# Kernel tuning notes

Measured on AMD Instinct MI355X. Metric: run time of the kernel, lower is better.

Reference implementation:

```python
import jax, jax.numpy as jnp
import numpy as np

B, S_WP, D_BERT = 64, 512, 768
NUM_WORDS = 256   # max words per sentence (segment count for scatter-mean)
H = 256           # LSTM hidden dim
A_MAX, K_MAX = 8, 4
N_LABELS = 4


def setup_inputs() -> dict:
    key = jax.random.key(0)
    ks = jax.random.split(key, 16)
    s = lambda shape, k, scale=0.05: jax.random.normal(k, shape, jnp.float32) * scale
    inp = {
        "embeddings": jax.random.normal(ks[0], (B, S_WP, D_BERT), jnp.float32),
        "mask": jnp.sort(jax.random.randint(ks[1], (B, S_WP), 0, NUM_WORDS), axis=-1),
        "aspect_idxs": jax.random.randint(ks[2], (B, A_MAX, K_MAX), 0, NUM_WORDS - 2),
        "w_ih_f": s((4 * H, D_BERT), ks[3]),
        "w_hh_f": s((4 * H, H), ks[4]),
        "b_ih_f": s((4 * H,), ks[5]),
        "b_hh_f": s((4 * H,), ks[6]),
        "w_ih_r": s((4 * H, D_BERT), ks[7]),
        "w_hh_r": s((4 * H, H), ks[8]),
        "b_ih_r": s((4 * H,), ks[9]),
        "b_hh_r": s((4 * H,), ks[10]),
        "fc1_w": s((H, 4 * H), ks[11]),
        "fc1_b": s((H,), ks[12]),
        "fc2_w": s((N_LABELS, H), ks[13]),
        "fc2_b": s((N_LABELS,), ks[14]),
    }
    return inp


def _lstm_dir(x, w_ih, w_hh, b_ih, b_hh, reverse):
    # x: [B, S, D] -> [B, S, H]; PyTorch gate order i, f, g, o.
    b, _, _ = x.shape
    h_dim = w_hh.shape[1]
    xg = jnp.einsum('bsd,gd->bsg', x, w_ih) + b_ih  # precompute input gates

    def step(carry, xg_t):
        h, c = carry
        g = xg_t + h @ w_hh.T + b_hh
        i, f, gg, o = jnp.split(g, 4, axis=-1)
        c = jax.nn.sigmoid(f) * c + jax.nn.sigmoid(i) * jnp.tanh(gg)
        h = jax.nn.sigmoid(o) * jnp.tanh(c)
        return (h, c), h

    init = (jnp.zeros((b, h_dim), x.dtype), jnp.zeros((b, h_dim), x.dtype))
    _, hs = jax.lax.scan(step, init, xg.transpose(1, 0, 2), reverse=reverse)
    return hs.transpose(1, 0, 2)


def _forward(embeddings, mask, aspect_idxs, w_ih_f, w_hh_f, b_ih_f, b_hh_f,
             w_ih_r, w_hh_r, b_ih_r, b_hh_r, fc1_w, fc1_b, fc2_w, fc2_b):
    # batch_scatter_mean: pool wordpieces into words via segment mean.
    seg_sum = jax.vmap(lambda e, m: jax.ops.segment_sum(e, m, num_segments=NUM_WORDS))(embeddings, mask)
    cnt = jax.vmap(lambda m: jax.ops.segment_sum(jnp.ones(m.shape, embeddings.dtype), m, num_segments=NUM_WORDS))(mask)
    words = seg_sum / jnp.maximum(cnt, 1.0)[..., None]  # [B, NUM_WORDS, D_BERT]

    # Bidirectional LSTM (dropout is identity in eval).
    h_f = _lstm_dir(words, w_ih_f, w_hh_f, b_ih_f, b_hh_f, reverse=False)
    h_r = _lstm_dir(words, w_ih_r, w_hh_r, b_ih_r, b_hh_r, reverse=True)
    out = jnp.concatenate([h_f, h_r], axis=-1)  # [B, S_words, 2H]

    b, s, hd = out.shape
    sent_mean = out.mean(axis=1)  # [B, 2H] (mean over full padded sequence, as original)

    # Ragged aspect gather-mean: sent_out[idxs + 1].mean(0), -1 pads masked out.
    tok_valid = (aspect_idxs >= 0).astype(out.dtype)              # [B, A, K]
    idx = jnp.clip(aspect_idxs, 0, s - 2) + 1                     # [B, A, K]
    gathered = jnp.take_along_axis(out, idx.reshape(b, -1, 1), axis=1)  # [B, A*K, 2H]
    gathered = gathered.reshape(b, A_MAX, K_MAX, hd)
    n_tok = tok_valid.sum(-1)                                     # [B, A]
    asp_mean = (gathered * tok_valid[..., None]).sum(2) / jnp.maximum(n_tok, 1.0)[..., None]

    valid = (n_tok > 0)[..., None]
    sent_b = jnp.broadcast_to(sent_mean[:, None, :], (b, A_MAX, hd))
    emb = jnp.where(valid, jnp.concatenate([sent_b, asp_mean], axis=-1), 0.0)  # [B, A, 4H]

    flat = emb.reshape(b * A_MAX, 2 * hd)
    h1 = jax.nn.relu(flat @ fc1_w.T + fc1_b)
    logits = h1 @ fc2_w.T + fc2_b
    return logits.reshape(b, A_MAX, -1)


def reference(embeddings, mask, aspect_idxs, w_ih_f, w_hh_f, b_ih_f, b_hh_f,
              w_ih_r, w_hh_r, b_ih_r, b_hh_r, fc1_w, fc1_b, fc2_w, fc2_b):
    return _forward(embeddings, mask, aspect_idxs, w_ih_f, w_hh_f, b_ih_f, b_hh_f,
                    w_ih_r, w_hh_r, b_ih_r, b_hh_r, fc1_w, fc1_b, fc2_w, fc2_b)
```

## Files before the change

kernel.cpp:

```cpp
#include <hip/hip_runtime.h>
#include <hip/hip_bf16.h>
#include <hip/hip_fp16.h>

#define B_   64
#define SWP  512
#define D_   768
#define W_   256
#define H_   256
#define G4   1024
#define N2   2048
#define M_   16384
#define A_   8
#define KK_  4

typedef __attribute__((ext_vector_type(4))) float f32x4;
typedef __attribute__((ext_vector_type(8))) short bf16x8;
typedef _Float16 __attribute__((ext_vector_type(2))) h2_t;

#define KR2 100
#define NCH 14

__device__ __forceinline__ void gload_lds16(const void* g, void* l) {
  __builtin_amdgcn_global_load_lds((const __attribute__((address_space(1))) void*)g,
                                   (__attribute__((address_space(3))) void*)l, 16, 0, 0);
}

__device__ __forceinline__ float sigm(float x) { return 1.f / (1.f + __expf(-x)); }
__device__ __forceinline__ float tanh_(float x) { return 1.f - 2.f / (1.f + __expf(2.f * x)); }

__device__ __forceinline__ float dot2acc(h2_t w, h2_t h, float acc) {
#if __has_builtin(__builtin_amdgcn_fdot2)
  return __builtin_amdgcn_fdot2(w, h, acc, false);
#else
  return acc + (float)w[0] * (float)h[0] + (float)w[1] * (float)h[1];
#endif
}

__device__ __forceinline__ h2_t bc_h2(unsigned int v) {
  union { unsigned int u; h2_t h; } cvt;
  cvt.u = v;
  return cvt.h;
}

__global__ __launch_bounds__(256) void k_words(const float* __restrict__ emb,
                                               const int* __restrict__ mask,
                                               __hip_bfloat16* __restrict__ words) {
  const int b = blockIdx.x >> 8;
  const int w = blockIdx.x & 255;
  const int tid = threadIdx.x;
  __shared__ int m[SWP];
  m[tid] = mask[b * SWP + tid];
  m[tid + 256] = mask[b * SWP + 256 + tid];
  __syncthreads();
  int lo = 0, hi = SWP;
  while (lo < hi) { int mid = (lo + hi) >> 1; if (m[mid] < w) lo = mid + 1; else hi = mid; }
  int lo2 = lo, hi2 = SWP;
  while (lo2 < hi2) { int mid = (lo2 + hi2) >> 1; if (m[mid] < w + 1) lo2 = mid + 1; else hi2 = mid; }
  const int cnt = lo2 - lo;
  const float inv = (cnt > 0) ? 1.f / (float)cnt : 0.f;
  float s0 = 0.f, s1 = 0.f, s2 = 0.f;
  for (int s = lo; s < lo2; ++s) {
    const float* row = emb + ((size_t)b * SWP + s) * D_;
    s0 += row[tid]; s1 += row[tid + 256]; s2 += row[tid + 512];
  }
  __hip_bfloat16* o = words + ((size_t)b * W_ + w) * D_;
  o[tid]       = __float2bfloat16(s0 * inv);
  o[tid + 256] = __float2bfloat16(s1 * inv);
  o[tid + 512] = __float2bfloat16(s2 * inv);
}

__global__ __launch_bounds__(256) void k_prep_wih(const float* __restrict__ wf, const float* __restrict__ wr,
                                                  const float* __restrict__ bihf, const float* __restrict__ bhhf,
                                                  const float* __restrict__ bihr, const float* __restrict__ bhhr,
                                                  __hip_bfloat16* __restrict__ wih, float* __restrict__ bias) {
  const int i = blockIdx.x * 256 + threadIdx.x;
  const int n = i / D_;
  const int k = i - n * D_;
  const float v = (n < G4) ? wf[n * D_ + k] : wr[(n - G4) * D_ + k];
  wih[i] = __float2bfloat16(v);
  if (i < N2) {
    bias[i] = (i < G4) ? (bihf[i] + bhhf[i]) : (bihr[i - G4] + bhhr[i - G4]);
  }
}

__global__ __launch_bounds__(256) void k_prep_whh(const float* __restrict__ whf,
                                                  const float* __restrict__ whr,
                                                  h2_t* __restrict__ whhP) {
  const int i = blockIdx.x * 256 + threadIdx.x;
  const int d = i >> 17;
  const int kk = (i >> 10) & 127;
  const int r = i & 1023;
  const float* w = d ? whr : whf;
  h2_t v;
  v[0] = (_Float16)w[r * H_ + 2 * kk];
  v[1] = (_Float16)w[r * H_ + 2 * kk + 1];
  whhP[i] = v;
}

__global__ __launch_bounds__(256) void k_gemm_xg(const __hip_bfloat16* __restrict__ A,
                                                 const __hip_bfloat16* __restrict__ Wt,
                                                 const float* __restrict__ bias,
                                                 _Float16* __restrict__ C) {
  const int bm = blockIdx.y * 128;
  const int bn = blockIdx.x * 128;
  __shared__ __hip_bfloat16 As[128 * 32];
  __shared__ __hip_bfloat16 Bs[128 * 32];
  const int tid = threadIdx.x;
  const int lane = tid & 63;
  const int wave = tid >> 6;
  const int wm = (wave >> 1) * 64;
  const int wn = (wave & 1) * 64;
  const int l15 = lane & 15;
  const int l4 = lane >> 4;
  const int row_a = tid >> 2;
  const int chunk = tid & 3;
  f32x4 acc[4][4] = {};
  for (int k0 = 0; k0 < D_; k0 += 32) {
    const __hip_bfloat16* ga  = A  + (size_t)(bm + row_a) * D_ + k0 + chunk * 8;
    const __hip_bfloat16* ga2 = A  + (size_t)(bm + 64 + row_a) * D_ + k0 + chunk * 8;
    const __hip_bfloat16* gb  = Wt + (size_t)(bn + row_a) * D_ + k0 + chunk * 8;
    const __hip_bfloat16* gb2 = Wt + (size_t)(bn + 64 + row_a) * D_ + k0 + chunk * 8;
    gload_lds16(ga,  As + tid * 8);
    gload_lds16(ga2, As + 2048 + tid * 8);
    gload_lds16(gb,  Bs + tid * 8);
    gload_lds16(gb2, Bs + 2048 + tid * 8);
    __syncthreads();
    bf16x8 af[4], bf[4];
#pragma unroll
    for (int i = 0; i < 4; ++i) {
      af[i] = *(const bf16x8*)(As + (wm + i * 16 + l15) * 32 + l4 * 8);
      bf[i] = *(const bf16x8*)(Bs + (wn + i * 16 + l15) * 32 + l4 * 8);
    }
#pragma unroll
    for (int i = 0; i < 4; ++i)
#pragma unroll
      for (int j = 0; j < 4; ++j)
        acc[i][j] = __builtin_amdgcn_mfma_f32_16x16x32_bf16(af[i], bf[j], acc[i][j], 0, 0, 0);
    __syncthreads();
  }
#pragma unroll
  for (int i = 0; i < 4; ++i) {
    const int m = bm + wm + i * 16 + l4 * 4;
#pragma unroll
    for (int j = 0; j < 4; ++j) {
      const int n = bn + wn + j * 16 + l15;
      const float bs = bias[n];
#pragma unroll
      for (int r = 0; r < 4; ++r)
        C[(size_t)(m + r) * N2 + n] = (_Float16)(acc[i][j][r] + bs);
    }
  }
}

__global__ __launch_bounds__(512)
__attribute__((amdgpu_waves_per_eu(2, 2)))
void k_lstm(const _Float16* __restrict__ xg,
            const h2_t* __restrict__ whhP,
            float* __restrict__ out) {
  const int bx = blockIdx.x;
  const int d = bx & 1;
  const int b = bx >> 1;
  const int t = threadIdx.x;
  const int u = t & 255;
  const bool low = (t < 256);
  const int r1 = low ? u : (256 + u);
  const int r2 = r1 + 512;

  __shared__ __align__(16) _Float16 hbuf[256];
  __shared__ __align__(16) h2_t wlds[NCH][512][4];
  __shared__ float fo[256][2];

  const h2_t* wp = whhP + (size_t)d * (128 * 1024);

  unsigned wr1[KR2], wr2[KR2];
#pragma unroll
  for (int kk = 0; kk < KR2; ++kk) {
    wr1[kk] = *(const unsigned*)&wp[kk * 1024 + r1];
    wr2[kk] = *(const unsigned*)&wp[kk * 1024 + r2];
  }
#pragma unroll
  for (int kk = 0; kk < KR2; ++kk) {
    asm volatile("" : "+v"(wr1[kk]));
    asm volatile("" : "+v"(wr2[kk]));
  }

#pragma unroll
  for (int c = 0; c < NCH; ++c) {
    const int row = (c < 7) ? r1 : r2;
    const int kb = KR2 + (c % 7) * 4;
    f32x4 v;
#pragma unroll
    for (int q = 0; q < 4; ++q)
      ((h2_t*)&v)[q] = wp[(kb + q) * 1024 + row];
    *(f32x4*)&wlds[c][t][0] = v;
  }
  if (t < 256) hbuf[t] = (_Float16)0.f;
  __syncthreads();

  float c_state = 0.f;
#pragma unroll 1
  for (int step = 0; step < W_; ++step) {
    const int tt = d ? (W_ - 1 - step) : step;
    const _Float16* xrow = xg + ((size_t)b * W_ + tt) * N2 + d * G4;
    const float xv1 = (float)xrow[r1];
    const float xv2 = (float)xrow[r2];
    float a1a = 0.f, a1b = 0.f, a2a = 0.f, a2b = 0.f;
    if (step > 0) {
      const f32x4* hb4 = (const f32x4*)&hbuf[0];
#pragma unroll
      for (int c = 0; c < 25; ++c) {
        const f32x4 hv = hb4[c];
        const h2_t* hp = (const h2_t*)&hv;
        a1a = dot2acc(bc_h2(wr1[c * 4 + 0]), hp[0], a1a);
        a1b = dot2acc(bc_h2(wr1[c * 4 + 1]), hp[1], a1b);
        a2a = dot2acc(bc_h2(wr2[c * 4 + 0]), hp[0], a2a);
        a2b = dot2acc(bc_h2(wr2[c * 4 + 1]), hp[1], a2b);
        a1a = dot2acc(bc_h2(wr1[c * 4 + 2]), hp[2], a1a);
        a1b = dot2acc(bc_h2(wr1[c * 4 + 3]), hp[3], a1b);
        a2a = dot2acc(bc_h2(wr2[c * 4 + 2]), hp[2], a2a);
        a2b = dot2acc(bc_h2(wr2[c * 4 + 3]), hp[3], a2b);
      }
#pragma unroll
      for (int j = 0; j < 7; ++j) {
        const f32x4 hv = hb4[25 + j];
        const f32x4 w1v = *(const f32x4*)&wlds[j][t][0];
        const f32x4 w2v = *(const f32x4*)&wlds[7 + j][t][0];
        const h2_t* hp = (const h2_t*)&hv;
        const h2_t* w1p = (const h2_t*)&w1v;
        const h2_t* w2p = (const h2_t*)&w2v;
        a1a = dot2acc(w1p[0], hp[0], a1a);
        a1b = dot2acc(w1p[1], hp[1], a1b);
        a2a = dot2acc(w2p[0], hp[0], a2a);
        a2b = dot2acc(w2p[1], hp[1], a2b);
        a1a = dot2acc(w1p[2], hp[2], a1a);
        a1b = dot2acc(w1p[3], hp[3], a1b);
        a2a = dot2acc(w2p[2], hp[2], a2a);
        a2b = dot2acc(w2p[3], hp[3], a2b);
      }
    }
    const float a1 = a1a + a1b + xv1;
    const float a2 = a2a + a2b + xv2;
    if (!low) { fo[u][0] = a1; fo[u][1] = a2; }
    __syncthreads();
    if (low) {
      const float ig = sigm(a1);
      const float gg = tanh_(a2);
      const float fg = sigm(fo[u][0]);
      const float og = sigm(fo[u][1]);
      c_state = fg * c_state + ig * gg;
      const float h = og * tanh_(c_state);
      out[((size_t)b * W_ + tt) * 512 + d * 256 + u] = h;
      hbuf[u] = (_Float16)h;
    }
    __syncthreads();
  }
}

__global__ __launch_bounds__(256) void k_head(const float* __restrict__ out,
                                              const int* __restrict__ aidx,
                                              const float* __restrict__ fc1w,
                                              const float* __restrict__ fc1b,
                                              const float* __restrict__ fc2w,
                                              const float* __restrict__ fc2b,
                                              float* __restrict__ logits) {
  const int b = blockIdx.x;
  const int t = threadIdx.x;
  __shared__ float emb[A_][1024];
  __shared__ float h1[A_][256];
  __shared__ float sent[512];
  const float* ob = out + (size_t)b * W_ * 512;
  float s0 = 0.f, s1 = 0.f;
  for (int tt = 0; tt < W_; ++tt) {
    s0 += ob[tt * 512 + t];
    s1 += ob[tt * 512 + 256 + t];
  }
  sent[t] = s0 * (1.f / 256.f);
  sent[t + 256] = s1 * (1.f / 256.f);
  __syncthreads();
  for (int a = 0; a < A_; ++a) {
    int nv = 0;
    float m0 = 0.f, m1 = 0.f;
    for (int k = 0; k < KK_; ++k) {
      const int idx = aidx[(b * A_ + a) * KK_ + k];
      if (idx >= 0) {
        const int tt = min(idx, W_ - 2) + 1;
        m0 += ob[tt * 512 + t];
        m1 += ob[tt * 512 + 256 + t];
        nv++;
      }
    }
    const float inv = nv > 0 ? 1.f / (float)nv : 0.f;
    const bool valid = nv > 0;
    emb[a][t]        = valid ? sent[t] : 0.f;
    emb[a][t + 256]  = valid ? sent[t + 256] : 0.f;
    emb[a][512 + t]       = m0 * inv;
    emb[a][512 + 256 + t] = m1 * inv;
  }
  __syncthreads();
  {
    float acc[A_];
#pragma unroll
    for (int a = 0; a < A_; ++a) acc[a] = fc1b[t];
    const float* wrow = fc1w + (size_t)t * 1024;
    for (int j = 0; j < 1024; j += 4) {
      const float4 w = *(const float4*)(wrow + j);
#pragma unroll
      for (int a = 0; a < A_; ++a) {
        const float4 e = *(const float4*)(&emb[a][j]);
        acc[a] += w.x * e.x + w.y * e.y + w.z * e.z + w.w * e.w;
      }
    }
#pragma unroll
    for (int a = 0; a < A_; ++a) h1[a][t] = fmaxf(acc[a], 0.f);
  }
  __syncthreads();
  if (t < A_ * 4) {
    const int a = t >> 2, l = t & 3;
    float acc = fc2b[l];
    const float* w = fc2w + l * 256;
    for (int j = 0; j < 256; ++j) acc += w[j] * h1[a][j];
    logits[(b * A_ + a) * 4 + l] = acc;
  }
}

extern "C" void kernel_launch(void* const* d_in, const int* in_sizes, int n_in,
                              void* d_out, int out_size, void* d_ws, size_t ws_size,
                              hipStream_t stream) {
  const float* emb  = (const float*)d_in[0];
  const int*   mask = (const int*)d_in[1];
  const int*   aidx = (const int*)d_in[2];
  const float* wihf = (const float*)d_in[3];
  const float* whhf = (const float*)d_in[4];
  const float* bihf = (const float*)d_in[5];
  const float* bhhf = (const float*)d_in[6];
  const float* wihr = (const float*)d_in[7];
  const float* whhr = (const float*)d_in[8];
  const float* bihr = (const float*)d_in[9];
  const float* bhhr = (const float*)d_in[10];
  const float* fc1w = (const float*)d_in[11];
  const float* fc1b = (const float*)d_in[12];
  const float* fc2w = (const float*)d_in[13];
  const float* fc2b = (const float*)d_in[14];
  float* logits = (float*)d_out;

  char* ws = (char*)d_ws;
  size_t off = 0;
  auto alloc = [&](size_t bytes) -> void* {
    void* p = ws + off;
    off += (bytes + 255) & ~(size_t)255;
    return p;
  };
  __hip_bfloat16* words = (__hip_bfloat16*)alloc((size_t)M_ * D_ * 2);
  _Float16*       xg    = (_Float16*)alloc((size_t)M_ * N2 * 2);
  __hip_bfloat16* wih   = (__hip_bfloat16*)alloc((size_t)N2 * D_ * 2);
  float*          bias  = (float*)alloc((size_t)N2 * 4);
  h2_t*           whhP  = (h2_t*)alloc((size_t)2 * 128 * 1024 * 4);
  float*          outh  = (float*)alloc((size_t)B_ * W_ * 512 * 4);

  k_words<<<B_ * W_, 256, 0, stream>>>(emb, mask, words);
  k_prep_wih<<<(N2 * D_) / 256, 256, 0, stream>>>(wihf, wihr, bihf, bhhf, bihr, bhhr, wih, bias);
  k_prep_whh<<<(2 * 128 * 1024) / 256, 256, 0, stream>>>(whhf, whhr, whhP);
  dim3 gg(N2 / 128, M_ / 128);
  k_gemm_xg<<<gg, 256, 0, stream>>>(words, wih, bias, xg);
  k_lstm<<<B_ * 2, 512, 0, stream>>>(xg, whhP, outh);
  k_head<<<B_, 256, 0, stream>>>(outh, aidx, fc1w, fc1b, fc2w, fc2b, logits);
}
```

Measured before the change: 659.7 us.

## Hold recurrent weights in AGPRs and broadcast hidden state via readlane

The LSTM recurrent kernel now keeps 96 of 128 packed weight pairs per row in accumulation registers (AGPRs) instead of VGPRs, and moves the rest to a larger LDS staging array. The hidden state is no longer read from LDS as 16-byte vectors. Each lane loads one packed pair, and the values are broadcast with readlane into scalar operands for the dot products. This targets LDS read traffic and VGPR pressure on the per-step critical path. The cost is an extra accvgpr read per weight and serialized readlane instructions.

Measured after the change: 2.064 ms. 213% more time.

```diff
diff --git a/kernel.cpp b/kernel.cpp
--- a/kernel.cpp
+++ b/kernel.cpp
@@ -17,8 +17,8 @@
 typedef __attribute__((ext_vector_type(8))) short bf16x8;
 typedef _Float16 __attribute__((ext_vector_type(2))) h2_t;
 
-#define KR2 100
-#define NCH 14
+#define KA2 96
+#define KL2 32
 
 __device__ __forceinline__ void gload_lds16(const void* g, void* l) {
   __builtin_amdgcn_global_load_lds((const __attribute__((address_space(1))) void*)g,
@@ -162,32 +162,30 @@
   const int b = bx >> 1;
   const int t = threadIdx.x;
   const int u = t & 255;
+  const int l = t & 63;
   const bool low = (t < 256);
   const int r1 = low ? u : (256 + u);
   const int r2 = r1 + 512;
 
   __shared__ __align__(16) _Float16 hbuf[256];
-  __shared__ __align__(16) h2_t wlds[NCH][512][4];
+  __shared__ __align__(16) h2_t wlds[16][512][4];
   __shared__ float fo[256][2];
 
   const h2_t* wp = whhP + (size_t)d * (128 * 1024);
 
-  unsigned wr1[KR2], wr2[KR2];
-#pragma unroll
-  for (int kk = 0; kk < KR2; ++kk) {
-    wr1[kk] = *(const unsigned*)&wp[kk * 1024 + r1];
-    wr2[kk] = *(const unsigned*)&wp[kk * 1024 + r2];
-  }
-#pragma unroll
-  for (int kk = 0; kk < KR2; ++kk) {
-    asm volatile("" : "+v"(wr1[kk]));
-    asm volatile("" : "+v"(wr2[kk]));
-  }
-
-#pragma unroll
-  for (int c = 0; c < NCH; ++c) {
-    const int row = (c < 7) ? r1 : r2;
-    const int kb = KR2 + (c % 7) * 4;
+  unsigned ag1[KA2], ag2[KA2];
+#pragma unroll
+  for (int kk = 0; kk < KA2; ++kk) {
+    unsigned t1 = *(const unsigned*)&wp[kk * 1024 + r1];
+    unsigned t2 = *(const unsigned*)&wp[kk * 1024 + r2];
+    asm volatile("v_accvgpr_write_b32 %0, %1" : "=a"(ag1[kk]) : "v"(t1));
+    asm volatile("v_accvgpr_write_b32 %0, %1" : "=a"(ag2[kk]) : "v"(t2));
+  }
+
+#pragma unroll
+  for (int c = 0; c < 16; ++c) {
+    const int row = (c < 8) ? r1 : r2;
+    const int kb = KA2 + (c & 7) * 4;
     f32x4 v;
 #pragma unroll
     for (int q = 0; q < 4; ++q)
@@ -206,36 +204,53 @@
     const float xv2 = (float)xrow[r2];
     float a1a = 0.f, a1b = 0.f, a2a = 0.f, a2b = 0.f;
     if (step > 0) {
-      const f32x4* hb4 = (const f32x4*)&hbuf[0];
-#pragma unroll
-      for (int c = 0; c < 25; ++c) {
-        const f32x4 hv = hb4[c];
-        const h2_t* hp = (const h2_t*)&hv;
-        a1a = dot2acc(bc_h2(wr1[c * 4 + 0]), hp[0], a1a);
-        a1b = dot2acc(bc_h2(wr1[c * 4 + 1]), hp[1], a1b);
-        a2a = dot2acc(bc_h2(wr2[c * 4 + 0]), hp[0], a2a);
-        a2b = dot2acc(bc_h2(wr2[c * 4 + 1]), hp[1], a2b);
-        a1a = dot2acc(bc_h2(wr1[c * 4 + 2]), hp[2], a1a);
-        a1b = dot2acc(bc_h2(wr1[c * 4 + 3]), hp[3], a1b);
-        a2a = dot2acc(bc_h2(wr2[c * 4 + 2]), hp[2], a2a);
-        a2b = dot2acc(bc_h2(wr2[c * 4 + 3]), hp[3], a2b);
-      }
-#pragma unroll
-      for (int j = 0; j < 7; ++j) {
-        const f32x4 hv = hb4[25 + j];
+      const unsigned hA = *(const unsigned*)&hbuf[2 * l];
+      const unsigned hB = *(const unsigned*)&hbuf[128 + 2 * l];
+#pragma unroll
+      for (int k = 0; k < 64; k += 2) {
+        unsigned w1a, w2a, w1b, w2b;
+        asm volatile("v_accvgpr_read_b32 %0, %1" : "=v"(w1a) : "a"(ag1[k]));
+        asm volatile("v_accvgpr_read_b32 %0, %1" : "=v"(w2a) : "a"(ag2[k]));
+        const h2_t h0 = bc_h2(__builtin_amdgcn_readlane(hA, k));
+        a1a = dot2acc(bc_h2(w1a), h0, a1a);
+        a2a = dot2acc(bc_h2(w2a), h0, a2a);
+        asm volatile("v_accvgpr_read_b32 %0, %1" : "=v"(w1b) : "a"(ag1[k + 1]));
+        asm volatile("v_accvgpr_read_b32 %0, %1" : "=v"(w2b) : "a"(ag2[k + 1]));
+        const h2_t h1 = bc_h2(__builtin_amdgcn_readlane(hA, k + 1));
+        a1b = dot2acc(bc_h2(w1b), h1, a1b);
+        a2b = dot2acc(bc_h2(w2b), h1, a2b);
+      }
+#pragma unroll
+      for (int k = 0; k < 32; k += 2) {
+        unsigned w1a, w2a, w1b, w2b;
+        asm volatile("v_accvgpr_read_b32 %0, %1" : "=v"(w1a) : "a"(ag1[64 + k]));
+        asm volatile("v_accvgpr_read_b32 %0, %1" : "=v"(w2a) : "a"(ag2[64 + k]));
+        const h2_t h0 = bc_h2(__builtin_amdgcn_readlane(hB, k));
+        a1a = dot2acc(bc_h2(w1a), h0, a1a);
+        a2a = dot2acc(bc_h2(w2a), h0, a2a);
+        asm volatile("v_accvgpr_read_b32 %0, %1" : "=v"(w1b) : "a"(ag1[64 + k + 1]));
+        asm volatile("v_accvgpr_read_b32 %0, %1" : "=v"(w2b) : "a"(ag2[64 + k + 1]));
+        const h2_t h1 = bc_h2(__builtin_amdgcn_readlane(hB, k + 1));
+        a1b = dot2acc(bc_h2(w1b), h1, a1b);
+        a2b = dot2acc(bc_h2(w2b), h1, a2b);
+      }
+#pragma unroll
+      for (int j = 0; j < 8; ++j) {
         const f32x4 w1v = *(const f32x4*)&wlds[j][t][0];
-        const f32x4 w2v = *(const f32x4*)&wlds[7 + j][t][0];
-        const h2_t* hp = (const h2_t*)&hv;
+        const f32x4 w2v = *(const f32x4*)&wlds[8 + j][t][0];
         const h2_t* w1p = (const h2_t*)&w1v;
         const h2_t* w2p = (const h2_t*)&w2v;
-        a1a = dot2acc(w1p[0], hp[0], a1a);
-        a1b = dot2acc(w1p[1], hp[1], a1b);
-        a2a = dot2acc(w2p[0], hp[0], a2a);
-        a2b = dot2acc(w2p[1], hp[1], a2b);
-        a1a = dot2acc(w1p[2], hp[2], a1a);
-        a1b = dot2acc(w1p[3], hp[3], a1b);
-        a2a = dot2acc(w2p[2], hp[2], a2a);
-        a2b = dot2acc(w2p[3], hp[3], a2b);
+#pragma unroll
+        for (int q = 0; q < 4; ++q) {
+          const h2_t hq = bc_h2(__builtin_amdgcn_readlane(hB, 32 + j * 4 + q));
+          if (q & 1) {
+            a1b = dot2acc(w1p[q], hq, a1b);
+            a2b = dot2acc(w2p[q], hq, a2b);
+          } else {
+            a1a = dot2acc(w1p[q], hq, a1a);
+            a2a = dot2acc(w2p[q], hq, a2a);
+          }
+        }
       }
     }
     const float a1 = a1a + a1b + xv1;
```
